# Optimization experiments

Hardware: AMD Instinct MI355X
Metric: run time of the kernel (lower is better)

The kernel has to match this reference:

```python
import jax, jax.numpy as jnp
import numpy as np

EPS = 1e-5  # haiku LayerNorm default


def _layernorm_last(x, scale, offset):
    m = jnp.mean(x, axis=-1, keepdims=True)
    v = jnp.var(x, axis=-1, keepdims=True)
    return (x - m) * jax.lax.rsqrt(v + EPS) * scale + offset


def setup_inputs() -> dict:
    key = jax.random.key(0)
    ks = jax.random.split(key, 6)
    N, C = 512, 128
    return {
        "act": jax.random.normal(ks[0], (N, N, C), dtype=jnp.float32),
        "mask": jnp.ones((N, N), dtype=jnp.float32),
        "ln_scale": jnp.ones((C,), dtype=jnp.float32),
        "ln_offset": jnp.zeros((C,), dtype=jnp.float32),
        "w_proj": jax.random.normal(ks[1], (C, 2 * C), dtype=jnp.float32) * 0.02,
        "w_gate": jax.random.normal(ks[2], (C, 2 * C), dtype=jnp.float32) * 0.02,
        "cn_scale": jnp.ones((C,), dtype=jnp.float32),
        "cn_offset": jnp.zeros((C,), dtype=jnp.float32),
        "w_out": jax.random.normal(ks[3], (C, C), dtype=jnp.float32) * 0.02,
        "b_out": jnp.zeros((C,), dtype=jnp.float32),
        "w_gate_out": jax.random.normal(ks[4], (C, C), dtype=jnp.float32) * 0.02,
        "b_gate_out": jnp.ones((C,), dtype=jnp.float32),  # bias_init=1.0
    }


def reference(act, mask, ln_scale, ln_offset, w_proj, w_gate,
              cn_scale, cn_offset, w_out, b_out, w_gate_out, b_gate_out):
    C = act.shape[-1]
    # left_norm_input (LayerNorm over channel axis)
    x = _layernorm_last(act, ln_scale, ln_offset)  # [N,N,C]
    input_act = x
    # gated linear unit: projection * sigmoid(gate), no biases (GLU kernel path)
    proj = jnp.einsum('ijc,cd->ijd', x, w_proj) * jax.nn.sigmoid(
        jnp.einsum('ijc,cd->ijd', x, w_gate))  # [N,N,2C]
    proj = jnp.transpose(proj, (2, 0, 1)) * mask[None]  # [2C,N,N]
    # split even/odd channels: reshape(C,2,N,N) -> a=proj[:,0], b=proj[:,1]
    proj = proj.reshape(C, 2, *proj.shape[1:])
    a, b = proj[:, 0], proj[:, 1]  # each [C,N,N]
    # triangle einsum ('ikc,jkc->ijc' -> 'cik,cjk->cij')
    act2 = jnp.einsum('cik,cjk->cij', a, b)  # [C,N,N]
    # center_norm: LayerNorm over channel axis (axis=0), params on axis 0
    m = jnp.mean(act2, axis=0, keepdims=True)
    v = jnp.var(act2, axis=0, keepdims=True)
    act2 = (act2 - m) * jax.lax.rsqrt(v + EPS) * cn_scale[:, None, None] + cn_offset[:, None, None]
    out = jnp.transpose(act2, (1, 2, 0))  # [N,N,C]
    out = jnp.einsum('ijc,cd->ijd', out, w_out) + b_out
    gate_out = jax.nn.sigmoid(jnp.einsum('ijc,cd->ijd', input_act, w_gate_out) + b_gate_out)
    return out * gate_out
```

## Files before the change

kernel.cpp:

```cpp
#include <hip/hip_runtime.h>
#include <stdint.h>

#define NDIM 512
#define CDIM 128
#define MDIM (NDIM*NDIM)

typedef unsigned short u16;
typedef __bf16 bf16v8 __attribute__((ext_vector_type(8)));
typedef float f32x4 __attribute__((ext_vector_type(4)));
typedef short s16x4 __attribute__((ext_vector_type(4)));

__device__ __forceinline__ u16 f2bf(float f){
  union { float f; uint32_t u; } v; v.f = f;
  uint32_t u = v.u;
  u += 0x7fffu + ((u >> 16) & 1u);
  return (u16)(u >> 16);
}
__device__ __forceinline__ float bf2f(u16 h){
  union { uint32_t u; float f; } v; v.u = ((uint32_t)h) << 16;
  return v.f;
}
__device__ __forceinline__ float sigm(float x){
  return __builtin_amdgcn_rcpf(1.0f + __expf(-x));
}
__device__ __forceinline__ f32x4 mfma_bf16(bf16v8 a, bf16v8 b, f32x4 c){
  return __builtin_amdgcn_mfma_f32_16x16x32_bf16(a, b, c, 0, 0, 0);
}

__global__ void k0_prep(const float* __restrict__ wp, const float* __restrict__ wg,
                        const float* __restrict__ wgo, const float* __restrict__ wo,
                        u16* __restrict__ wt){
  const int d = blockIdx.x, k = threadIdx.x;
  float v;
  if (d < 256)      v = wp[k*256 + d];
  else if (d < 512) v = wg[k*256 + (d-256)];
  else if (d < 640) v = wgo[k*128 + (d-512)];
  else              v = wo[k*128 + (d-640)];
  wt[d*CDIM + k] = f2bf(v);
}

__global__ __launch_bounds__(256) void k1_ln_proj(
    const float* __restrict__ act, const float* __restrict__ mask,
    const float* __restrict__ lns, const float* __restrict__ lno,
    const u16* __restrict__ wt, u16* __restrict__ AB)
{
  __shared__ __align__(16) u16 xs[64][136];
  __shared__ __align__(16) u16 pgs[256][72];
  __shared__ float msk[64];
  const int t = threadIdx.x;
  const int blk = ((int)blockIdx.x & 7)*512 + ((int)blockIdx.x >> 3);
  const int m0 = blk * 64;

  {
    const int r = t >> 2, q = t & 3;
    const float4* rp = (const float4*)(act + (size_t)(m0 + r)*CDIM + q*32);
    float4 v[8];
    #pragma unroll
    for (int i = 0; i < 8; ++i) v[i] = rp[i];
    float s = 0.f, s2 = 0.f;
    #pragma unroll
    for (int i = 0; i < 8; ++i){
      s  += v[i].x + v[i].y + v[i].z + v[i].w;
      s2 += v[i].x*v[i].x + v[i].y*v[i].y + v[i].z*v[i].z + v[i].w*v[i].w;
    }
    s += __shfl_xor(s, 1);  s2 += __shfl_xor(s2, 1);
    s += __shfl_xor(s, 2);  s2 += __shfl_xor(s2, 2);
    const float mean = s * (1.f/128.f);
    const float rstd = rsqrtf(s2 * (1.f/128.f) - mean*mean + 1e-5f);
    const float4* lsp = (const float4*)(lns + q*32);
    const float4* lop = (const float4*)(lno + q*32);
    #pragma unroll
    for (int i = 0; i < 8; ++i){
      const float4 sc = lsp[i], of = lop[i];
      s16x4 pk;
      pk.x = (short)f2bf((v[i].x - mean)*rstd*sc.x + of.x);
      pk.y = (short)f2bf((v[i].y - mean)*rstd*sc.y + of.y);
      pk.z = (short)f2bf((v[i].z - mean)*rstd*sc.z + of.z);
      pk.w = (short)f2bf((v[i].w - mean)*rstd*sc.w + of.w);
      *(s16x4*)&xs[r][q*32 + i*4] = pk;
    }
    if (t < 64) msk[t] = mask[m0 + t];
  }
  __syncthreads();

  const int w = t >> 6, L = t & 63, ln16 = L & 15, quad = L >> 4;
  bf16v8 af[4][4];
  #pragma unroll
  for (int rs = 0; rs < 4; ++rs)
    #pragma unroll
    for (int kk = 0; kk < 4; ++kk)
      af[rs][kk] = *(const bf16v8*)&xs[rs*16 + ln16][kk*32 + quad*8];

  const f32x4 zero4 = {0.f,0.f,0.f,0.f};
  #pragma unroll
  for (int pp = 0; pp < 4; ++pp){
    const int p = w*4 + pp;
    const u16* wpr = wt + (size_t)(16*p + ln16)*CDIM + quad*8;
    const u16* wgr = wpr + (size_t)256*CDIM;
    bf16v8 bp[4], bg[4];
    #pragma unroll
    for (int kk = 0; kk < 4; ++kk){
      bp[kk] = *(const bf16v8*)(wpr + kk*32);
      bg[kk] = *(const bf16v8*)(wgr + kk*32);
    }
    f32x4 aP[4] = {zero4, zero4, zero4, zero4};
    f32x4 aG[4] = {zero4, zero4, zero4, zero4};
    #pragma unroll
    for (int kk = 0; kk < 4; ++kk)
      #pragma unroll
      for (int rs = 0; rs < 4; ++rs){
        aP[rs] = mfma_bf16(af[rs][kk], bp[kk], aP[rs]);
        aG[rs] = mfma_bf16(af[rs][kk], bg[kk], aG[rs]);
      }
    #pragma unroll
    for (int rs = 0; rs < 4; ++rs)
      #pragma unroll
      for (int reg = 0; reg < 4; ++reg){
        const int ml = rs*16 + quad*4 + reg;
        const float pg = aP[rs][reg] * sigm(aG[rs][reg]) * msk[ml];
        pgs[16*p + ln16][ml] = f2bf(pg);
      }
  }
  __syncthreads();

  #pragma unroll
  for (int p4 = 0; p4 < 4; ++p4){
    const int d = p4*64 + (t >> 2), q = t & 3;
    u16* dst = AB + (size_t)d*MDIM + m0 + q*16;
    const u16* src = &pgs[d][q*16];
    *(bf16v8*)dst       = *(const bf16v8*)src;
    *(bf16v8*)(dst + 8) = *(const bf16v8*)(src + 8);
  }
}

__global__ __launch_bounds__(256) void k2_tri(const u16* __restrict__ AB,
                                              u16* __restrict__ act2)
{
  __shared__ __align__(16) u16 As[128][72];
  __shared__ __align__(16) u16 Bs[128][72];
  const int t = threadIdx.x;
  const int bid = ((int)blockIdx.x & 7)*256 + ((int)blockIdx.x >> 3);
  const int c  = bid >> 4;
  const int i0 = ((bid >> 2) & 3) * 128;
  const int j0 = (bid & 3) * 128;
  const u16* Ag = AB + (size_t)(2*c)*MDIM;
  const u16* Bg = AB + (size_t)(2*c + 1)*MDIM;

  const int w = t >> 6, L = t & 63, ln16 = L & 15, quad = L >> 4;
  const int iw = (w & 1)*64, jw = (w >> 1)*64;
  const int r = t >> 1, h = t & 1;

  const f32x4 zero4 = {0.f,0.f,0.f,0.f};
  f32x4 acc[4][4];
  #pragma unroll
  for (int x = 0; x < 4; ++x)
    #pragma unroll
    for (int y = 0; y < 4; ++y) acc[x][y] = zero4;

  for (int k0 = 0; k0 < NDIM; k0 += 64){
    const u16* ga = Ag + (size_t)(i0 + r)*NDIM + k0 + h*32;
    const u16* gb = Bg + (size_t)(j0 + r)*NDIM + k0 + h*32;
    bf16v8 sa[4], sb[4];
    #pragma unroll
    for (int x = 0; x < 4; ++x){
      sa[x] = *(const bf16v8*)(ga + x*8);
      sb[x] = *(const bf16v8*)(gb + x*8);
    }
    __syncthreads();
    #pragma unroll
    for (int x = 0; x < 4; ++x){
      *(bf16v8*)&As[r][h*32 + x*8] = sa[x];
      *(bf16v8*)&Bs[r][h*32 + x*8] = sb[x];
    }
    __syncthreads();
    #pragma unroll
    for (int kk = 0; kk < 2; ++kk){
      bf16v8 ar[4], br[4];
      #pragma unroll
      for (int x = 0; x < 4; ++x) ar[x] = *(const bf16v8*)&As[iw + x*16 + ln16][kk*32 + quad*8];
      #pragma unroll
      for (int y = 0; y < 4; ++y) br[y] = *(const bf16v8*)&Bs[jw + y*16 + ln16][kk*32 + quad*8];
      #pragma unroll
      for (int x = 0; x < 4; ++x)
        #pragma unroll
        for (int y = 0; y < 4; ++y)
          acc[x][y] = mfma_bf16(ar[x], br[y], acc[x][y]);
    }
  }

  u16* op = act2 + (size_t)c*MDIM;
  #pragma unroll
  for (int x = 0; x < 4; ++x)
    #pragma unroll
    for (int y = 0; y < 4; ++y)
      #pragma unroll
      for (int reg = 0; reg < 4; ++reg){
        const int il = iw + x*16 + quad*4 + reg;
        const int jl = jw + y*16 + ln16;
        op[(size_t)(i0 + il)*NDIM + j0 + jl] = f2bf(acc[x][y][reg]);
      }
}

__global__ __launch_bounds__(256) void k3_out(
    const u16* __restrict__ act2, const u16* __restrict__ wt,
    const float* __restrict__ act,
    const float* __restrict__ lns, const float* __restrict__ lno,
    const float* __restrict__ cns, const float* __restrict__ cno,
    const float* __restrict__ bo, const float* __restrict__ bgo,
    float* __restrict__ out)
{
  __shared__ __align__(16) u16 vs[128*74];
  const int t = threadIdx.x;
  const int blk = ((int)blockIdx.x & 7)*512 + ((int)blockIdx.x >> 3);
  const int i  = blk >> 3;
  const int j0 = (blk & 7)*64;
  const int m0 = i*NDIM + j0;

  const int w = t >> 6, L = t & 63, ln16 = L & 15, quad = L >> 4;

  const int arow = m0 + w*16 + ln16;
  float4 av[8];
  #pragma unroll
  for (int kk = 0; kk < 4; ++kk){
    const float* ap = act + (size_t)arow*CDIM + kk*32 + quad*8;
    av[2*kk]   = *(const float4*)(ap);
    av[2*kk+1] = *(const float4*)(ap + 4);
  }

  {
    const int cc = t >> 1, h = t & 1;
    const u16* g = act2 + (size_t)cc*MDIM + (size_t)i*NDIM + j0 + h*32;
    #pragma unroll
    for (int x = 0; x < 4; ++x)
      *(bf16v8*)&vs[cc*74 + h*32 + x*8] = *(const bf16v8*)(g + x*8);
  }

  union bfu { bf16v8 v; u16 u[8]; };
  bf16v8 ag[4];
  {
    float s = 0.f, s2 = 0.f;
    #pragma unroll
    for (int q2 = 0; q2 < 8; ++q2){
      s  += av[q2].x + av[q2].y + av[q2].z + av[q2].w;
      s2 += av[q2].x*av[q2].x + av[q2].y*av[q2].y + av[q2].z*av[q2].z + av[q2].w*av[q2].w;
    }
    s += __shfl_xor(s,16); s2 += __shfl_xor(s2,16);
    s += __shfl_xor(s,32); s2 += __shfl_xor(s2,32);
    const float mean = s*(1.f/128.f);
    const float rstd = rsqrtf(s2*(1.f/128.f) - mean*mean + 1e-5f);
    #pragma unroll
    for (int kk = 0; kk < 4; ++kk){
      const float4 sc0 = *(const float4*)(lns + kk*32 + quad*8);
      const float4 sc1 = *(const float4*)(lns + kk*32 + quad*8 + 4);
      const float4 of0 = *(const float4*)(lno + kk*32 + quad*8);
      const float4 of1 = *(const float4*)(lno + kk*32 + quad*8 + 4);
      bfu pk;
      pk.u[0] = f2bf((av[2*kk].x   - mean)*rstd*sc0.x + of0.x);
      pk.u[1] = f2bf((av[2*kk].y   - mean)*rstd*sc0.y + of0.y);
      pk.u[2] = f2bf((av[2*kk].z   - mean)*rstd*sc0.z + of0.z);
      pk.u[3] = f2bf((av[2*kk].w   - mean)*rstd*sc0.w + of0.w);
      pk.u[4] = f2bf((av[2*kk+1].x - mean)*rstd*sc1.x + of1.x);
      pk.u[5] = f2bf((av[2*kk+1].y - mean)*rstd*sc1.y + of1.y);
      pk.u[6] = f2bf((av[2*kk+1].z - mean)*rstd*sc1.z + of1.z);
      pk.u[7] = f2bf((av[2*kk+1].w - mean)*rstd*sc1.w + of1.w);
      ag[kk] = pk.v;
    }
  }
  __syncthreads();

  bf16v8 af[4];
  {
    const int jj = w*16 + ln16;
    float cv[32];
    float s = 0.f, s2 = 0.f;
    #pragma unroll
    for (int kk = 0; kk < 4; ++kk)
      #pragma unroll
      for (int e = 0; e < 8; ++e){
        const float v = bf2f(vs[(kk*32 + quad*8 + e)*74 + jj]);
        cv[kk*8 + e] = v; s += v; s2 += v*v;
      }
    s += __shfl_xor(s,16); s2 += __shfl_xor(s2,16);
    s += __shfl_xor(s,32); s2 += __shfl_xor(s2,32);
    const float mean = s*(1.f/128.f);
    const float rstd = rsqrtf(s2*(1.f/128.f) - mean*mean + 1e-5f);
    #pragma unroll
    for (int kk = 0; kk < 4; ++kk){
      const float4 sc0 = *(const float4*)(cns + kk*32 + quad*8);
      const float4 sc1 = *(const float4*)(cns + kk*32 + quad*8 + 4);
      const float4 of0 = *(const float4*)(cno + kk*32 + quad*8);
      const float4 of1 = *(const float4*)(cno + kk*32 + quad*8 + 4);
      bfu pk;
      pk.u[0] = f2bf((cv[kk*8+0] - mean)*rstd*sc0.x + of0.x);
      pk.u[1] = f2bf((cv[kk*8+1] - mean)*rstd*sc0.y + of0.y);
      pk.u[2] = f2bf((cv[kk*8+2] - mean)*rstd*sc0.z + of0.z);
      pk.u[3] = f2bf((cv[kk*8+3] - mean)*rstd*sc0.w + of0.w);
      pk.u[4] = f2bf((cv[kk*8+4] - mean)*rstd*sc1.x + of1.x);
      pk.u[5] = f2bf((cv[kk*8+5] - mean)*rstd*sc1.y + of1.y);
      pk.u[6] = f2bf((cv[kk*8+6] - mean)*rstd*sc1.z + of1.z);
      pk.u[7] = f2bf((cv[kk*8+7] - mean)*rstd*sc1.w + of1.w);
      af[kk] = pk.v;
    }
  }

  const f32x4 zero4 = {0.f,0.f,0.f,0.f};
  #pragma unroll
  for (int n = 0; n < 8; ++n){
    const u16* wr  = wt + (size_t)(640 + n*16 + ln16)*CDIM + quad*8;
    const u16* wgr = wt + (size_t)(512 + n*16 + ln16)*CDIM + quad*8;
    bf16v8 bb[4], bg[4];
    #pragma unroll
    for (int kk = 0; kk < 4; ++kk){
      bb[kk] = *(const bf16v8*)(wr  + kk*32);
      bg[kk] = *(const bf16v8*)(wgr + kk*32);
    }
    f32x4 ao = zero4, agg = zero4;
    #pragma unroll
    for (int kk = 0; kk < 4; ++kk){
      ao  = mfma_bf16(af[kk], bb[kk], ao);
      agg = mfma_bf16(ag[kk], bg[kk], agg);
    }
    const int e = n*16 + ln16;
    const float bias = bo[e], bge = bgo[e];
    #pragma unroll
    for (int reg = 0; reg < 4; ++reg){
      const int jl = w*16 + quad*4 + reg;
      out[((size_t)(m0 + jl))*(size_t)CDIM + e] =
          (ao[reg] + bias) * sigm(agg[reg] + bge);
    }
  }
}

extern "C" void kernel_launch(void* const* d_in, const int* in_sizes, int n_in,
                              void* d_out, int out_size, void* d_ws, size_t ws_size,
                              hipStream_t stream)
{
  const float* act = (const float*)d_in[0];
  const float* msk = (const float*)d_in[1];
  const float* lns = (const float*)d_in[2];
  const float* lno = (const float*)d_in[3];
  const float* wp  = (const float*)d_in[4];
  const float* wg  = (const float*)d_in[5];
  const float* cns = (const float*)d_in[6];
  const float* cno = (const float*)d_in[7];
  const float* wo  = (const float*)d_in[8];
  const float* bo  = (const float*)d_in[9];
  const float* wgo = (const float*)d_in[10];
  const float* bgo = (const float*)d_in[11];
  float* out = (float*)d_out;

  u16* AB   = (u16*)d_ws;
  u16* ACT2 = AB + (size_t)256*MDIM;
  u16* WT   = ACT2 + (size_t)128*MDIM;

  k0_prep   <<<dim3(768),  dim3(128), 0, stream>>>(wp, wg, wgo, wo, WT);
  k1_ln_proj<<<dim3(4096), dim3(256), 0, stream>>>(act, msk, lns, lno, WT, AB);
  k2_tri    <<<dim3(2048), dim3(256), 0, stream>>>(AB, ACT2);
  k3_out    <<<dim3(4096), dim3(256), 0, stream>>>(ACT2, WT, act, lns, lno,
                                                   cns, cno, bo, bgo, out);
}
```

Measured before the change: 558.2 us.

## Make k3_out persistent over four tiles with double-buffered LDS prefetch

The output kernel now handles four consecutive 64-column tiles per block instead of one, with a quarter as many blocks. While one tile computes, the next tile's act2 gather and act rows are prefetched into registers, then stored to a second LDS buffer. The centre-norm values are reread from LDS rather than held in a 32-float register array. The aim is to hide global load latency and amortise block setup, at the cost of more registers and LDS per block, which may lower occupancy.

```diff
diff --git a/kernel.cpp b/kernel.cpp
--- a/kernel.cpp
+++ b/kernel.cpp
@@ -209,35 +209,40 @@
     const float* __restrict__ bo, const float* __restrict__ bgo,
     float* __restrict__ out)
 {
-  __shared__ __align__(16) u16 vs[128*74];
+  __shared__ __align__(16) u16 vs[2][128*74];
   const int t = threadIdx.x;
-  const int blk = ((int)blockIdx.x & 7)*512 + ((int)blockIdx.x >> 3);
-  const int i  = blk >> 3;
-  const int j0 = (blk & 7)*64;
-  const int m0 = i*NDIM + j0;
-
+  const int sblk = ((int)blockIdx.x & 7)*128 + ((int)blockIdx.x >> 3);
+  const int i   = sblk >> 1;
+  const int jb0 = (sblk & 1)*4;
   const int w = t >> 6, L = t & 63, ln16 = L & 15, quad = L >> 4;
-
-  const int arow = m0 + w*16 + ln16;
+  const int cc = t >> 1, hh = t & 1;
+  const u16* gbase = act2 + (size_t)cc*MDIM + (size_t)i*NDIM + jb0*64 + hh*32;
+
+  union bfu { bf16v8 v; u16 u[8]; };
+  bf16v8 ag[2][4];
   float4 av[8];
-  #pragma unroll
-  for (int kk = 0; kk < 4; ++kk){
-    const float* ap = act + (size_t)arow*CDIM + kk*32 + quad*8;
-    av[2*kk]   = *(const float4*)(ap);
-    av[2*kk+1] = *(const float4*)(ap + 4);
-  }
-
-  {
-    const int cc = t >> 1, h = t & 1;
-    const u16* g = act2 + (size_t)cc*MDIM + (size_t)i*NDIM + j0 + h*32;
+  bf16v8 gv[4];
+
+  auto load_gather = [&](int tt){
     #pragma unroll
     for (int x = 0; x < 4; ++x)
-      *(bf16v8*)&vs[cc*74 + h*32 + x*8] = *(const bf16v8*)(g + x*8);
-  }
-
-  union bfu { bf16v8 v; u16 u[8]; };
-  bf16v8 ag[4];
-  {
+      gv[x] = *(const bf16v8*)(gbase + tt*64 + x*8);
+  };
+  auto load_av = [&](int tt){
+    const int arow = i*NDIM + (jb0 + tt)*64 + w*16 + ln16;
+    #pragma unroll
+    for (int kk = 0; kk < 4; ++kk){
+      const float* ap = act + (size_t)arow*CDIM + kk*32 + quad*8;
+      av[2*kk]   = *(const float4*)(ap);
+      av[2*kk+1] = *(const float4*)(ap + 4);
+    }
+  };
+  auto store_gather = [&](int buf){
+    #pragma unroll
+    for (int x = 0; x < 4; ++x)
+      *(bf16v8*)&vs[buf][cc*74 + hh*32 + x*8] = gv[x];
+  };
+  auto make_ag = [&](bf16v8* dst){
     float s = 0.f, s2 = 0.f;
     #pragma unroll
     for (int q2 = 0; q2 < 8; ++q2){
@@ -263,22 +268,18 @@
       pk.u[5] = f2bf((av[2*kk+1].y - mean)*rstd*sc1.y + of1.y);
       pk.u[6] = f2bf((av[2*kk+1].z - mean)*rstd*sc1.z + of1.z);
       pk.u[7] = f2bf((av[2*kk+1].w - mean)*rstd*sc1.w + of1.w);
-      ag[kk] = pk.v;
-    }
-  }
-  __syncthreads();
-
-  bf16v8 af[4];
-  {
+      dst[kk] = pk.v;
+    }
+  };
+  auto make_af = [&](const u16* vsb, bf16v8* dst){
     const int jj = w*16 + ln16;
-    float cv[32];
     float s = 0.f, s2 = 0.f;
     #pragma unroll
     for (int kk = 0; kk < 4; ++kk)
       #pragma unroll
       for (int e = 0; e < 8; ++e){
-        const float v = bf2f(vs[(kk*32 + quad*8 + e)*74 + jj]);
-        cv[kk*8 + e] = v; s += v; s2 += v*v;
+        const float v = bf2f(vsb[(kk*32 + quad*8 + e)*74 + jj]);
+        s += v; s2 += v*v;
       }
     s += __shfl_xor(s,16); s2 += __shfl_xor(s2,16);
     s += __shfl_xor(s,32); s2 += __shfl_xor(s2,32);
@@ -291,42 +292,71 @@
       const float4 of0 = *(const float4*)(cno + kk*32 + quad*8);
       const float4 of1 = *(const float4*)(cno + kk*32 + quad*8 + 4);
       bfu pk;
-      pk.u[0] = f2bf((cv[kk*8+0] - mean)*rstd*sc0.x + of0.x);
-      pk.u[1] = f2bf((cv[kk*8+1] - mean)*rstd*sc0.y + of0.y);
-      pk.u[2] = f2bf((cv[kk*8+2] - mean)*rstd*sc0.z + of0.z);
-      pk.u[3] = f2bf((cv[kk*8+3] - mean)*rstd*sc0.w + of0.w);
-      pk.u[4] = f2bf((cv[kk*8+4] - mean)*rstd*sc1.x + of1.x);
-      pk.u[5] = f2bf((cv[kk*8+5] - mean)*rstd*sc1.y + of1.y);
-      pk.u[6] = f2bf((cv[kk*8+6] - mean)*rstd*sc1.z + of1.z);
-      pk.u[7] = f2bf((cv[kk*8+7] - mean)*rstd*sc1.w + of1.w);
-      af[kk] = pk.v;
-    }
-  }
+      #pragma unroll
+      for (int e = 0; e < 4; ++e){
+        const float v = bf2f(vsb[(kk*32 + quad*8 + e)*74 + jj]);
+        const float sc = (e==0)?sc0.x:(e==1)?sc0.y:(e==2)?sc0.z:sc0.w;
+        const float of = (e==0)?of0.x:(e==1)?of0.y:(e==2)?of0.z:of0.w;
+        pk.u[e] = f2bf((v - mean)*rstd*sc + of);
+      }
+      #pragma unroll
+      for (int e = 0; e < 4; ++e){
+        const float v = bf2f(vsb[(kk*32 + quad*8 + 4 + e)*74 + jj]);
+        const float sc = (e==0)?sc1.x:(e==1)?sc1.y:(e==2)?sc1.z:sc1.w;
+        const float of = (e==0)?of1.x:(e==1)?of1.y:(e==2)?of1.z:of1.w;
+        pk.u[4+e] = f2bf((v - mean)*rstd*sc + of);
+      }
+      dst[kk] = pk.v;
+    }
+  };
+
+  load_gather(0);
+  load_av(0);
+  store_gather(0);
+  make_ag(ag[0]);
+  __syncthreads();
 
   const f32x4 zero4 = {0.f,0.f,0.f,0.f};
   #pragma unroll
-  for (int n = 0; n < 8; ++n){
-    const u16* wr  = wt + (size_t)(640 + n*16 + ln16)*CDIM + quad*8;
-    const u16* wgr = wt + (size_t)(512 + n*16 + ln16)*CDIM + quad*8;
-    bf16v8 bb[4], bg[4];
-    #pragma unroll
-    for (int kk = 0; kk < 4; ++kk){
-      bb[kk] = *(const bf16v8*)(wr  + kk*32);
-      bg[kk] = *(const bf16v8*)(wgr + kk*32);
-    }
-    f32x4 ao = zero4, agg = zero4;
-    #pragma unroll
-    for (int kk = 0; kk < 4; ++kk){
-      ao  = mfma_bf16(af[kk], bb[kk], ao);
-      agg = mfma_bf16(ag[kk], bg[kk], agg);
-    }
-    const int e = n*16 + ln16;
-    const float bias = bo[e], bge = bgo[e];
-    #pragma unroll
-    for (int reg = 0; reg < 4; ++reg){
-      const int jl = w*16 + quad*4 + reg;
-      out[((size_t)(m0 + jl))*(size_t)CDIM + e] =
-          (ao[reg] + bias) * sigm(agg[reg] + bge);
+  for (int tt = 0; tt < 4; ++tt){
+    if (tt < 3){
+      load_gather(tt + 1);
+      load_av(tt + 1);
+    }
+    bf16v8 af[4];
+    make_af(vs[tt & 1], af);
+
+    const int m0 = i*NDIM + (jb0 + tt)*64;
+    #pragma unroll
+    for (int n = 0; n < 8; ++n){
+      const u16* wr  = wt + (size_t)(640 + n*16 + ln16)*CDIM + quad*8;
+      const u16* wgr = wt + (size_t)(512 + n*16 + ln16)*CDIM + quad*8;
+      bf16v8 bb[4], bg[4];
+      #pragma unroll
+      for (int kk = 0; kk < 4; ++kk){
+        bb[kk] = *(const bf16v8*)(wr  + kk*32);
+        bg[kk] = *(const bf16v8*)(wgr + kk*32);
+      }
+      f32x4 ao = zero4, agg = zero4;
+      #pragma unroll
+      for (int kk = 0; kk < 4; ++kk){
+        ao  = mfma_bf16(af[kk], bb[kk], ao);
+        agg = mfma_bf16(ag[tt & 1][kk], bg[kk], agg);
+      }
+      const int e = n*16 + ln16;
+      const float bias = bo[e], bge = bgo[e];
+      #pragma unroll
+      for (int reg = 0; reg < 4; ++reg){
+        const int jl = w*16 + quad*4 + reg;
+        out[((size_t)(m0 + jl))*(size_t)CDIM + e] =
+            (ao[reg] + bias) * sigm(agg[reg] + bge);
+      }
+    }
+
+    if (tt < 3){
+      store_gather((tt + 1) & 1);
+      make_ag(ag[(tt + 1) & 1]);
+      __syncthreads();
     }
   }
 }
@@ -356,6 +386,6 @@
   k0_prep   <<<dim3(768),  dim3(128), 0, stream>>>(wp, wg, wgo, wo, WT);
   k1_ln_proj<<<dim3(4096), dim3(256), 0, stream>>>(act, msk, lns, lno, WT, AB);
   k2_tri    <<<dim3(2048), dim3(256), 0, stream>>>(AB, ACT2);
-  k3_out    <<<dim3(4096), dim3(256), 0, stream>>>(ACT2, WT, act, lns, lno,
+  k3_out    <<<dim3(1024), dim3(256), 0, stream>>>(ACT2, WT, act, lns, lno,
                                                    cns, cno, bo, bgo, out);
 }
```

After: 611.8 us. 1.1x slower.
